# Kernel optimization log

Measured on AMD Instinct MI355X. Metric: run time of the kernel, lower is better.

The kernel has to match this reference:

```python
import jax, jax.numpy as jnp
import numpy as np

LN_EPS = 1e-5

def sin_emb(coords, dim):
    # coords [..., 3] -> [..., dim]; dim split evenly over 3 axes, sin/cos halves
    per_axis = dim // 3
    half = per_axis // 2
    freqs = jnp.exp(-jnp.log(10000.0) * jnp.arange(half, dtype=coords.dtype) / max(half - 1, 1))
    ang = coords[..., None] * freqs  # [..., 3, half]
    emb = jnp.concatenate([jnp.sin(ang), jnp.cos(ang)], axis=-1)  # [..., 3, per_axis]
    return emb.reshape(coords.shape[:-1] + (dim,))

def layernorm(x, g, b):
    mu = jnp.mean(x, axis=-1, keepdims=True)
    var = jnp.mean((x - mu) ** 2, axis=-1, keepdims=True)
    return (x - mu) * jax.lax.rsqrt(var + LN_EPS) * g + b

def point_mlp(x, w, b, g, be, act):
    h = layernorm(x @ w + b, g, be)
    return jax.nn.gelu(h, approximate=False) if act else h

def query_ball_point(radius, nsample, xyz):
    # xyz [B,N,3] -> idx [B,N,nsample] (pad with first in-ball index, PointNet++ style)
    N = xyz.shape[1]
    sq = jnp.sum((xyz[:, :, None, :] - xyz[:, None, :, :]) ** 2, axis=-1)  # [B,N,N]
    idx0 = jnp.where(sq > radius * radius, N, jnp.arange(N)[None, None, :])
    idx = jnp.sort(idx0, axis=-1)[:, :, :nsample]
    return jnp.where(idx == N, idx[:, :, :1], idx)

def index_points(points, idx):
    # points [B,N,C], idx [B,S,K] -> [B,S,K,C]
    return jax.vmap(lambda p, i: p[i])(points, idx)

def setup_inputs() -> dict:
    key = jax.random.key(0)
    ks = jax.random.split(key, 20)
    B, N, C_stem, C_tok = 4, 4096, 64, 256
    C_in = C_stem + 3 + 24 + 96  # 187
    w = lambda k, i, o: jax.random.normal(k, (i, o), jnp.float32) * 0.02
    inp = {
        'xyz': jax.random.uniform(ks[0], (B, N, 3), jnp.float32),
        'point_feature': jax.random.normal(ks[1], (B, N, C_stem), jnp.float32),
        # scene_point_mlp
        'w1': w(ks[2], C_in, C_tok), 'b1': jnp.zeros((C_tok,)), 'g1': jnp.ones((C_tok,)), 'be1': jnp.zeros((C_tok,)),
        'w2': w(ks[3], C_tok, C_tok), 'b2': jnp.zeros((C_tok,)), 'g2': jnp.ones((C_tok,)), 'be2': jnp.zeros((C_tok,)),
        # scene_projection
        'pw1': w(ks[4], C_tok, C_tok), 'pb1': jnp.zeros((C_tok,)), 'pg1': jnp.ones((C_tok,)), 'pbe1': jnp.zeros((C_tok,)),
        'pw2': w(ks[5], C_tok, C_tok), 'pb2': jnp.zeros((C_tok,)), 'pg2': jnp.ones((C_tok,)), 'pbe2': jnp.zeros((C_tok,)),
    }
    return inp

def reference(xyz, point_feature, w1, b1, g1, be1, w2, b2, g2, be2,
              pw1, pb1, pg1, pbe1, pw2, pb2, pg2, pbe2):
    radius, K = 0.16, 32
    idx = query_ball_point(radius, K, xyz)                     # [B,N,K]
    grouped_xyz = index_points(xyz, idx)                       # [B,N,K,3]
    grouped_feature = index_points(point_feature, idx)         # [B,N,K,Cs]
    relative_xyz = grouped_xyz - xyz[:, :, None, :]            # [B,N,K,3]
    relative_position = sin_emb(relative_xyz, 24)              # [B,N,K,24]
    absolute_position = sin_emb(xyz, 96)                       # [B,N,96]
    B, N = xyz.shape[0], xyz.shape[1]
    absolute_position = jnp.broadcast_to(absolute_position[:, :, None, :], (B, N, K, 96))
    grouped_input = jnp.concatenate(
        (grouped_feature, relative_xyz, relative_position, absolute_position), axis=-1)
    h = point_mlp(grouped_input, w1, b1, g1, be1, True)
    h = point_mlp(h, w2, b2, g2, be2, False)
    scene_point_feature = jnp.max(h, axis=2)                   # [B,N,C]
    pooled = jnp.max(scene_point_feature, axis=1, keepdims=True)  # [B,1,C]
    t = point_mlp(pooled, pw1, pb1, pg1, pbe1, True)
    global_scene_token = point_mlp(t, pw2, pb2, pg2, pbe2, False)
    return global_scene_token
```

## Files before the change

### kernel.cpp

```cpp
#include <hip/hip_runtime.h>
#include <hip/hip_bf16.h>
#include <math.h>


#define LN_EPS 1e-5f

typedef __attribute__((ext_vector_type(8))) short bf16x8;
typedef __attribute__((ext_vector_type(4))) float f32x4;
typedef __attribute__((ext_vector_type(2))) unsigned int u32x2;
typedef __attribute__((ext_vector_type(4))) unsigned int u32x4;

#if __has_builtin(__builtin_amdgcn_rcpf)
#define FRCP(x) __builtin_amdgcn_rcpf(x)
#else
#define FRCP(x) (1.0f / (x))
#endif

__device__ __forceinline__ unsigned short f2bf(float f) {
    unsigned int x = __float_as_uint(f);
    return (unsigned short)((x + 0x7FFFu + ((x >> 16) & 1u)) >> 16);
}
__device__ __forceinline__ unsigned int pack2(float a, float b) {
    union { __hip_bfloat162 h; unsigned int u; } cvt;
    cvt.h = __float22bfloat162_rn(make_float2(a, b));
    return cvt.u;
}
__device__ __forceinline__ unsigned int fenc(float f) {
    unsigned int u = __float_as_uint(f);
    return (u & 0x80000000u) ? ~u : (u | 0x80000000u);
}
__device__ __forceinline__ float fdec(unsigned int u) {
    return __uint_as_float((u & 0x80000000u) ? (u & 0x7FFFFFFFu) : ~u);
}
__device__ __forceinline__ float gelu_fast(float x) {
    float x2 = x * x;
    float u = x * fmaf(0.0356774081f, x2, 0.7978845608f);
    float e = exp2f(u * -2.8853900818f);
    float r = FRCP(e + 1.0f);
    return x * r;
}
template<int CTRL>
__device__ __forceinline__ float dppadd(float s) {
    int v = __builtin_amdgcn_update_dpp(0, __float_as_int(s), CTRL, 0xF, 0xF, true);
    return s + __int_as_float(v);
}
__device__ __forceinline__ float rowsum16(float x) {
    x = dppadd<0x128>(x);
    x = dppadd<0x124>(x);
    x = dppadd<0x122>(x);
    x = dppadd<0x121>(x);
    return x;
}

__global__ __launch_bounds__(256) void k_prep(
    const float* __restrict__ w1, const float* __restrict__ w2,
    unsigned short* __restrict__ w2T, unsigned short* __restrict__ w1aT,
    unsigned short* __restrict__ w1cT, unsigned short* __restrict__ w1bT,
    unsigned int* __restrict__ pooled_r)
{
    int t = threadIdx.x, blk = blockIdx.x;
    if (blk < 16) {
        __shared__ unsigned short tile[64][65];
        int tr = blk >> 2, tc = blk & 3;
        #pragma unroll
        for (int rr = 0; rr < 16; ++rr) {
            int kl = rr * 4 + (t >> 6), nl = t & 63;
            tile[kl][nl] = f2bf(w2[(size_t)(tr * 64 + kl) * 256 + tc * 64 + nl]);
        }
        __syncthreads();
        #pragma unroll
        for (int rr = 0; rr < 16; ++rr) {
            int nl = rr * 4 + (t >> 6), kp = t & 63;
            int kl = (kp & 3) * 16 + (kp >> 2);
            w2T[(size_t)(tc * 64 + nl) * 256 + tr * 64 + kp] = tile[kl][nl];
        }
    } else if (blk < 20) {
        __shared__ unsigned short tile[64][65];
        int tc = blk - 16;
        #pragma unroll
        for (int rr = 0; rr < 16; ++rr) {
            int kl = rr * 4 + (t >> 6), nl = t & 63;
            tile[kl][nl] = f2bf(w1[(size_t)kl * 256 + tc * 64 + nl]);
        }
        __syncthreads();
        #pragma unroll
        for (int rr = 0; rr < 16; ++rr) {
            int nl = rr * 4 + (t >> 6), kl = t & 63;
            w1aT[(size_t)(tc * 64 + nl) * 64 + kl] = tile[kl][nl];
        }
    } else if (blk < 28) {
        __shared__ unsigned short tile[64][65];
        int idx = blk - 20;
        int tr2 = idx >> 2, tc = idx & 3;
        #pragma unroll
        for (int rr = 0; rr < 16; ++rr) {
            int kl = rr * 4 + (t >> 6), nl = t & 63;
            int k = tr2 * 64 + kl;
            float v = 0.f;
            if (k < 96) v = w1[(size_t)(91 + k) * 256 + tc * 64 + nl];
            tile[kl][nl] = f2bf(v);
        }
        __syncthreads();
        #pragma unroll
        for (int rr = 0; rr < 16; ++rr) {
            int nl = rr * 4 + (t >> 6), kl = t & 63;
            int k = tr2 * 64 + kl;
            if (k < 96)
                w1cT[(size_t)(tc * 64 + nl) * 96 + k] = tile[kl][nl];
        }
    } else if (blk == 28) {
        int n = t;
        #pragma unroll
        for (int k = 0; k < 32; ++k) {
            unsigned short v = 0;
            if (k < 27) v = f2bf(w1[(size_t)(64 + k) * 256 + n]);
            w1bT[(size_t)n * 32 + k] = v;
        }
    } else {
        unsigned int idv = fenc(-1e19f);
        for (int q = t; q < 32768; q += 256) pooled_r[q] = idv;
    }
}

__global__ __launch_bounds__(256) void k_pre(
    const float* __restrict__ xyz, const float* __restrict__ pf,
    const unsigned short* __restrict__ w1aT, const unsigned short* __restrict__ w1cT,
    const float* __restrict__ b1,
    float* __restrict__ U_p, float* __restrict__ V_p)
{
    __shared__ __align__(16) unsigned short ptile[16 * 72];
    __shared__ __align__(16) unsigned short etile[16 * 104];
    int tid = threadIdx.x, wv = tid >> 6, lane = tid & 63;
    int lo16 = lane & 15, quad = lane >> 4;
    int rows0 = blockIdx.x * 16;

    {
        int r = tid >> 4, seg = tid & 15;
        f32x4 v = *(const f32x4*)(pf + (size_t)(rows0 + r) * 64 + seg * 4);
        u32x2 o; o.x = pack2(v.x, v.y); o.y = pack2(v.z, v.w);
        *(u32x2*)&ptile[r * 72 + seg * 4] = o;
    }
    #pragma unroll
    for (int q = 0; q < 3; ++q) {
        int item = q * 256 + tid;
        int r = item / 48, pr = item - 48 * r;
        float vals[2];
        #pragma unroll
        for (int qq = 0; qq < 2; ++qq) {
            int cc = pr * 2 + qq;
            int a = cc >> 5, wI = cc & 31;
            int jf = (wI < 16) ? wI : (wI - 16);
            float coord = xyz[(size_t)(rows0 + r) * 3 + a];
            float fr = __expf(-0.61402269146507894f * (float)jf);
            float ang = coord * fr;
            vals[qq] = (wI < 16) ? __sinf(ang) : __cosf(ang);
        }
        *(unsigned int*)&etile[r * 104 + 2 * pr] = pack2(vals[0], vals[1]);
    }
    __syncthreads();

    f32x4 acc[4];
    #pragma unroll
    for (int nt = 0; nt < 4; ++nt) acc[nt] = (f32x4){0.f, 0.f, 0.f, 0.f};
    #pragma unroll
    for (int ks = 0; ks < 2; ++ks) {
        bf16x8 afr = *(const bf16x8*)&ptile[lo16 * 72 + ks * 32 + quad * 8];
        #pragma unroll
        for (int nt = 0; nt < 4; ++nt) {
            int n = wv * 64 + nt * 16 + lo16;
            bf16x8 bfr = *(const bf16x8*)&w1aT[(size_t)n * 64 + ks * 32 + quad * 8];
            acc[nt] = __builtin_amdgcn_mfma_f32_16x16x32_bf16(afr, bfr, acc[nt], 0, 0, 0);
        }
    }
    #pragma unroll
    for (int reg = 0; reg < 4; ++reg) {
        f32x4 o = {acc[0][reg], acc[1][reg], acc[2][reg], acc[3][reg]};
        *(f32x4*)&U_p[(size_t)(rows0 + quad * 4 + reg) * 256 + wv * 64 + lo16 * 4] = o;
    }

    {
        float b1f[4];
        #pragma unroll
        for (int nt = 0; nt < 4; ++nt) b1f[nt] = b1[wv * 64 + nt * 16 + lo16];
        #pragma unroll
        for (int nt = 0; nt < 4; ++nt)
            #pragma unroll
            for (int reg = 0; reg < 4; ++reg) acc[nt][reg] = b1f[nt];
    }
    #pragma unroll
    for (int ks = 0; ks < 3; ++ks) {
        bf16x8 afr = *(const bf16x8*)&etile[lo16 * 104 + ks * 32 + quad * 8];
        #pragma unroll
        for (int nt = 0; nt < 4; ++nt) {
            int n = wv * 64 + nt * 16 + lo16;
            bf16x8 bfr = *(const bf16x8*)&w1cT[(size_t)n * 96 + ks * 32 + quad * 8];
            acc[nt] = __builtin_amdgcn_mfma_f32_16x16x32_bf16(afr, bfr, acc[nt], 0, 0, 0);
        }
    }
    #pragma unroll
    for (int reg = 0; reg < 4; ++reg) {
        f32x4 o = {acc[0][reg], acc[1][reg], acc[2][reg], acc[3][reg]};
        *(f32x4*)&V_p[(size_t)(rows0 + quad * 4 + reg) * 256 + wv * 64 + lo16 * 4] = o;
    }
}

__global__ __launch_bounds__(512, 4) void k_main(
    const float* __restrict__ xyz,
    const unsigned short* __restrict__ w1bT, const unsigned short* __restrict__ w2T,
    const float* __restrict__ U_p, const float* __restrict__ V_p,
    const float* __restrict__ g1, const float* __restrict__ be1,
    const float* __restrict__ b2, const float* __restrict__ g2,
    const float* __restrict__ be2,
    unsigned int* __restrict__ pooled_r)
{
    __shared__ __align__(16) unsigned short smem[128 * 264];
    __shared__ unsigned long long bmask[4][64];
    __shared__ int   idxs[128];
    __shared__ float ctr[4][3];
    __shared__ float reds[128][4][2];
    __shared__ float musig[128][2];
    __shared__ unsigned int pool_s[256];
    unsigned short* rels = smem;
    unsigned short* h1s  = smem;

    const int N = 4096;
    int tid = threadIdx.x, wv = tid >> 6, lane = tid & 63;
    int lo16 = lane & 15, quad = lane >> 4;
    int wvM = wv >> 2, wvN = wv & 3;
    int b = blockIdx.x & 3;
    int i0 = (blockIdx.x >> 2) * 4;
    int rep = (blockIdx.x >> 2) & 31;
    size_t base = (size_t)b * N;
    const float* xb = xyz + base * 3;

    bf16x8 bfrR[4];
    #pragma unroll
    for (int nt = 0; nt < 4; ++nt) {
        int n = wvN * 64 + nt * 16 + lo16;
        bfrR[nt] = *(const bf16x8*)&w1bT[(size_t)n * 32 + quad * 8];
    }

    if (tid < 256) pool_s[tid] = fenc(-1e19f);
    if (tid < 12) { int p = tid / 3, a = tid - 3 * p; ctr[p][a] = xb[(i0 + p) * 3 + a]; }
    const double r2d = 0.16 * 0.16;
    float T = (float)r2d;
    if ((double)T > r2d) T = __uint_as_float(__float_as_uint(T) - 1u);
    {
        f32x4 cA = *(const f32x4*)(xb + (size_t)i0 * 3);
        f32x4 cB = *(const f32x4*)(xb + (size_t)i0 * 3 + 4);
        f32x4 cC = *(const f32x4*)(xb + (size_t)i0 * 3 + 8);
        float cx0 = cA.x, cy0 = cA.y, cz0 = cA.z;
        float cx1 = cA.w, cy1 = cB.x, cz1 = cB.y;
        float cx2 = cB.z, cy2 = cB.w, cz2 = cC.x;
        float cx3 = cC.y, cy3 = cC.z, cz3 = cC.w;
        #pragma unroll 2
        for (int i = 0; i < 8; ++i) {
            int chunk = wv * 8 + i;
            int j = chunk * 64 + lane;
            const float* pp = xb + (size_t)j * 3;
            float px = pp[0], py = pp[1], pz = pp[2];
            float dx0 = __fsub_rn(px, cx0), dy0 = __fsub_rn(py, cy0), dz0 = __fsub_rn(pz, cz0);
            float sq0 = __fadd_rn(__fadd_rn(__fmul_rn(dx0, dx0), __fmul_rn(dy0, dy0)),
                                  __fmul_rn(dz0, dz0));
            unsigned long long m0 = __ballot(sq0 <= T);
            float dx1 = __fsub_rn(px, cx1), dy1 = __fsub_rn(py, cy1), dz1 = __fsub_rn(pz, cz1);
            float sq1 = __fadd_rn(__fadd_rn(__fmul_rn(dx1, dx1), __fmul_rn(dy1, dy1)),
                                  __fmul_rn(dz1, dz1));
            unsigned long long m1 = __ballot(sq1 <= T);
            float dx2 = __fsub_rn(px, cx2), dy2 = __fsub_rn(py, cy2), dz2 = __fsub_rn(pz, cz2);
            float sq2 = __fadd_rn(__fadd_rn(__fmul_rn(dx2, dx2), __fmul_rn(dy2, dy2)),
                                  __fmul_rn(dz2, dz2));
            unsigned long long m2 = __ballot(sq2 <= T);
            float dx3 = __fsub_rn(px, cx3), dy3 = __fsub_rn(py, cy3), dz3 = __fsub_rn(pz, cz3);
            float sq3 = __fadd_rn(__fadd_rn(__fmul_rn(dx3, dx3), __fmul_rn(dy3, dy3)),
                                  __fmul_rn(dz3, dz3));
            unsigned long long m3 = __ballot(sq3 <= T);
            if (lane == 0) {
                bmask[0][chunk] = m0; bmask[1][chunk] = m1;
                bmask[2][chunk] = m2; bmask[3][chunk] = m3;
            }
        }
    }
    __syncthreads();
    if (wv < 4) {
        int p = wv;
        unsigned long long m = bmask[p][lane];
        int c = __popcll(m);
        int inc = c;
        #pragma unroll
        for (int d = 1; d <= 32; d <<= 1) {
            int v = __shfl_up(inc, d);
            if (lane >= d) inc += v;
        }
        int exc = inc - c;
        int total = __shfl(inc, 63);
        unsigned long long lm = __ballot(m != 0ull);
        int fl = __ffsll(lm) - 1;
        unsigned long long mf = (unsigned long long)__shfl((long long)m, fl);
        int firstj = fl * 64 + __ffsll(mf) - 1;
        unsigned long long mm = m;
        int t = 0;
        while (mm != 0ull && (exc + t) < 32) {
            int bpos = __ffsll(mm) - 1;
            idxs[p * 32 + exc + t] = lane * 64 + bpos;
            mm &= mm - 1; ++t;
        }
        if (lane >= total && lane < 32) idxs[p * 32 + lane] = firstj;
    }
    __syncthreads();

    {
        int r = tid & 127, part = tid >> 7;
        int p = r >> 5;
        int j = idxs[r];
        float rx = xb[j * 3]     - ctr[p][0];
        float ry = xb[j * 3 + 1] - ctr[p][1];
        float rz = xb[j * 3 + 2] - ctr[p][2];
        unsigned short* arow = &rels[r * 40];
        if (part == 0) {
            *(unsigned int*)&arow[0] = pack2(rx, ry);
            arow[2] = f2bf(rz);
            arow[27] = 0;
            *(u32x2*)&arow[28] = (u32x2){0u, 0u};
        } else {
            int a = part - 1;
            float cv = (a == 0) ? rx : ((a == 1) ? ry : rz);
            const float fr4[4] = {1.f, 0.046415888336127774f,
                                  0.0021544346900318843f, 1e-4f};
            float sn[4], cs[4];
            #pragma unroll
            for (int tt = 0; tt < 4; ++tt) {
                float ang = cv * fr4[tt];
                sn[tt] = __sinf(ang); cs[tt] = __cosf(ang);
            }
            arow[3 + a * 8 + 0] = f2bf(sn[0]); arow[3 + a * 8 + 1] = f2bf(sn[1]);
            arow[3 + a * 8 + 2] = f2bf(sn[2]); arow[3 + a * 8 + 3] = f2bf(sn[3]);
            arow[3 + a * 8 + 4] = f2bf(cs[0]); arow[3 + a * 8 + 5] = f2bf(cs[1]);
            arow[3 + a * 8 + 6] = f2bf(cs[2]); arow[3 + a * 8 + 7] = f2bf(cs[3]);
        }
    }
    __syncthreads();

    const int arow0 = wvM * 64;
    f32x4 acc[4][4];
    #pragma unroll
    for (int mt = 0; mt < 4; ++mt) {
        int cl = wvM * 2 + (mt >> 1);
        f32x4 vv = *(const f32x4*)&V_p[(size_t)(base + i0 + cl) * 256 + wvN * 64 + lo16 * 4];
        #pragma unroll
        for (int reg = 0; reg < 4; ++reg) {
            int r = arow0 + mt * 16 + quad * 4 + reg;
            int j = idxs[r];
            f32x4 uu = *(const f32x4*)&U_p[(size_t)(base + j) * 256 + wvN * 64 + lo16 * 4];
            #pragma unroll
            for (int nt = 0; nt < 4; ++nt) acc[mt][nt][reg] = uu[nt] + vv[nt];
        }
    }
    #pragma unroll
    for (int mt = 0; mt < 4; ++mt) {
        bf16x8 afr = *(const bf16x8*)&rels[(arow0 + mt * 16 + lo16) * 40 + quad * 8];
        #pragma unroll
        for (int nt = 0; nt < 4; ++nt)
            acc[mt][nt] = __builtin_amdgcn_mfma_f32_16x16x32_bf16(
                afr, bfrR[nt], acc[mt][nt], 0, 0, 0);
    }

    #pragma unroll
    for (int mt = 0; mt < 4; ++mt) {
        #pragma unroll
        for (int reg = 0; reg < 4; ++reg) {
            float s1 = 0.f, s2 = 0.f;
            #pragma unroll
            for (int nt = 0; nt < 4; ++nt) { float v = acc[mt][nt][reg]; s1 += v; s2 = fmaf(v, v, s2); }
            s1 = rowsum16(s1); s2 = rowsum16(s2);
            if (lo16 == 0) {
                int r = arow0 + mt * 16 + quad * 4 + reg;
                reds[r][wvN][0] = s1; reds[r][wvN][1] = s2;
            }
        }
    }
    __syncthreads();
    if (tid < 128) {
        int r = tid;
        float s1 = reds[r][0][0] + reds[r][1][0] + reds[r][2][0] + reds[r][3][0];
        float s2 = reds[r][0][1] + reds[r][1][1] + reds[r][2][1] + reds[r][3][1];
        float mu = s1 * (1.f / 256.f);
        float var = fmaxf(s2 * (1.f / 256.f) - mu * mu, 0.f);
        musig[r][0] = mu; musig[r][1] = rsqrtf(var + LN_EPS);
    }
    __syncthreads();
    {
        float g1f[4], be1f[4];
        #pragma unroll
        for (int nt = 0; nt < 4; ++nt) {
            int n = wvN * 64 + nt * 16 + lo16;
            g1f[nt] = g1[n]; be1f[nt] = be1[n];
        }
        #pragma unroll
        for (int mt = 0; mt < 4; ++mt) {
            #pragma unroll
            for (int reg = 0; reg < 4; ++reg) {
                int r = arow0 + mt * 16 + quad * 4 + reg;
                float mu = musig[r][0], rs = musig[r][1];
                float v0 = gelu_fast(fmaf((acc[mt][0][reg] - mu) * rs, g1f[0], be1f[0]));
                float v1 = gelu_fast(fmaf((acc[mt][1][reg] - mu) * rs, g1f[1], be1f[1]));
                float v2 = gelu_fast(fmaf((acc[mt][2][reg] - mu) * rs, g1f[2], be1f[2]));
                float v3 = gelu_fast(fmaf((acc[mt][3][reg] - mu) * rs, g1f[3], be1f[3]));
                u32x2 w; w.x = pack2(v0, v1); w.y = pack2(v2, v3);
                *(u32x2*)&h1s[r * 264 + wvN * 64 + lo16 * 4] = w;
            }
        }
    }
    __syncthreads();

    {
        float b2f[4];
        #pragma unroll
        for (int nt = 0; nt < 4; ++nt) b2f[nt] = b2[wvN * 64 + nt * 16 + lo16];
        #pragma unroll
        for (int mt = 0; mt < 4; ++mt)
            #pragma unroll
            for (int nt = 0; nt < 4; ++nt)
                #pragma unroll
                for (int reg = 0; reg < 4; ++reg) acc[mt][nt][reg] = b2f[nt];
    }
    for (int ks = 0; ks < 8; ++ks) {
        bf16x8 bfr[4], afr[4];
        #pragma unroll
        for (int nt = 0; nt < 4; ++nt) {
            int n = wvN * 64 + nt * 16 + lo16;
            bfr[nt] = *(const bf16x8*)&w2T[(size_t)n * 256 + ks * 32 + quad * 8];
        }
        #pragma unroll
        for (int mt = 0; mt < 4; ++mt)
            afr[mt] = *(const bf16x8*)&h1s[(arow0 + mt * 16 + lo16) * 264 + ks * 32 + quad * 8];
        #pragma unroll
        for (int mt = 0; mt < 4; ++mt)
            #pragma unroll
            for (int nt = 0; nt < 4; ++nt)
                acc[mt][nt] = __builtin_amdgcn_mfma_f32_16x16x32_bf16(
                    afr[mt], bfr[nt], acc[mt][nt], 0, 0, 0);
    }

    {
        #pragma unroll
        for (int mt = 0; mt < 4; ++mt) {
            #pragma unroll
            for (int reg = 0; reg < 4; ++reg) {
                float s1 = 0.f, s2 = 0.f;
                #pragma unroll
                for (int nt = 0; nt < 4; ++nt) { float v = acc[mt][nt][reg]; s1 += v; s2 = fmaf(v, v, s2); }
                s1 = rowsum16(s1); s2 = rowsum16(s2);
                if (lo16 == 0) {
                    int r = arow0 + mt * 16 + quad * 4 + reg;
                    reds[r][wvN][0] = s1; reds[r][wvN][1] = s2;
                }
            }
        }
        __syncthreads();
        if (tid < 128) {
            int r = tid;
            float s1 = reds[r][0][0] + reds[r][1][0] + reds[r][2][0] + reds[r][3][0];
            float s2 = reds[r][0][1] + reds[r][1][1] + reds[r][2][1] + reds[r][3][1];
            float mu = s1 * (1.f / 256.f);
            float var = fmaxf(s2 * (1.f / 256.f) - mu * mu, 0.f);
            musig[r][0] = mu; musig[r][1] = rsqrtf(var + LN_EPS);
        }
        __syncthreads();

        float g2f[4], be2f[4];
        #pragma unroll
        for (int nt = 0; nt < 4; ++nt) {
            int n = wvN * 64 + nt * 16 + lo16;
            g2f[nt] = g2[n]; be2f[nt] = be2[n];
        }
        float mx[4] = {-1e30f, -1e30f, -1e30f, -1e30f};
        #pragma unroll
        for (int mt = 0; mt < 4; ++mt) {
            #pragma unroll
            for (int reg = 0; reg < 4; ++reg) {
                int r = arow0 + mt * 16 + quad * 4 + reg;
                float mu = musig[r][0], rs = musig[r][1];
                #pragma unroll
                for (int nt = 0; nt < 4; ++nt) {
                    float v = fmaf((acc[mt][nt][reg] - mu) * rs, g2f[nt], be2f[nt]);
                    mx[nt] = fmaxf(mx[nt], v);
                }
            }
        }
        #pragma unroll
        for (int nt = 0; nt < 4; ++nt) {
            mx[nt] = fmaxf(mx[nt], __shfl_xor(mx[nt], 16));
            mx[nt] = fmaxf(mx[nt], __shfl_xor(mx[nt], 32));
        }
        if (quad == 0) {
            #pragma unroll
            for (int nt = 0; nt < 4; ++nt)
                atomicMax(&pool_s[wvN * 64 + nt * 16 + lo16], fenc(mx[nt]));
        }
    }
    __syncthreads();
    if (tid < 256)
        atomicMax(pooled_r + rep * 1024 + b * 256 + tid, pool_s[tid]);
}

__global__ __launch_bounds__(256) void k_final(
    const unsigned int* __restrict__ pooled_r,
    const float* __restrict__ pw1, const float* __restrict__ pb1,
    const float* __restrict__ pg1, const float* __restrict__ pbe1,
    const float* __restrict__ pw2, const float* __restrict__ pb2,
    const float* __restrict__ pg2, const float* __restrict__ pbe2,
    float* __restrict__ out)
{
    __shared__ float xw[256], xh[256];
    __shared__ float lred[2][4];
    int tid = threadIdx.x, wv = tid >> 6;
    int bb = blockIdx.x;

    {
        unsigned int mv = pooled_r[bb * 256 + tid];
        #pragma unroll
        for (int r = 1; r < 32; ++r) {
            unsigned int v = pooled_r[r * 1024 + bb * 256 + tid];
            mv = (v > mv) ? v : mv;
        }
        xw[tid] = fdec(mv);
    }
    __syncthreads();

    float a1 = pb1[tid];
    #pragma unroll 8
    for (int k = 0; k < 256; ++k)
        a1 = fmaf(xw[k], pw1[(size_t)k * 256 + tid], a1);
    float s1 = a1, s2 = a1 * a1;
    s1 = rowsum16(s1); s2 = rowsum16(s2);
    s1 += __shfl_xor(s1, 16); s2 += __shfl_xor(s2, 16);
    s1 += __shfl_xor(s1, 32); s2 += __shfl_xor(s2, 32);
    if ((tid & 63) == 0) { lred[0][wv] = s1; lred[1][wv] = s2; }
    __syncthreads();
    s1 = lred[0][0] + lred[0][1] + lred[0][2] + lred[0][3];
    s2 = lred[1][0] + lred[1][1] + lred[1][2] + lred[1][3];
    float mu = s1 * (1.f / 256.f);
    float rs = rsqrtf(fmaxf(s2 * (1.f / 256.f) - mu * mu, 0.f) + LN_EPS);
    xh[tid] = gelu_fast(fmaf((a1 - mu) * rs, pg1[tid], pbe1[tid]));
    __syncthreads();

    float a2 = pb2[tid];
    #pragma unroll 8
    for (int k = 0; k < 256; ++k)
        a2 = fmaf(xh[k], pw2[(size_t)k * 256 + tid], a2);
    s1 = a2; s2 = a2 * a2;
    s1 = rowsum16(s1); s2 = rowsum16(s2);
    s1 += __shfl_xor(s1, 16); s2 += __shfl_xor(s2, 16);
    s1 += __shfl_xor(s1, 32); s2 += __shfl_xor(s2, 32);
    if ((tid & 63) == 0) { lred[0][wv] = s1; lred[1][wv] = s2; }
    __syncthreads();
    s1 = lred[0][0] + lred[0][1] + lred[0][2] + lred[0][3];
    s2 = lred[1][0] + lred[1][1] + lred[1][2] + lred[1][3];
    mu = s1 * (1.f / 256.f);
    rs = rsqrtf(fmaxf(s2 * (1.f / 256.f) - mu * mu, 0.f) + LN_EPS);
    out[bb * 256 + tid] = fmaf((a2 - mu) * rs, pg2[tid], pbe2[tid]);
}

extern "C" void kernel_launch(void* const* d_in, const int* in_sizes, int n_in,
                              void* d_out, int out_size, void* d_ws, size_t ws_size,
                              hipStream_t stream)
{
    char* ws = (char*)d_ws;
    unsigned short* w2T      = (unsigned short*)ws;
    unsigned short* w1aT     = (unsigned short*)(ws + (128u << 10));
    unsigned short* w1cT     = (unsigned short*)(ws + (160u << 10));
    unsigned short* w1bT     = (unsigned short*)(ws + (208u << 10));
    unsigned int*   pooled_r = (unsigned int*)(ws + (224u << 10));
    float*          U_p      = (float*)(ws + (512u << 10));
    float*          V_p      = (float*)(ws + (512u << 10) + (16u << 20));

    const float* xyz = (const float*)d_in[0];
    const float* pf  = (const float*)d_in[1];
    const float* w1  = (const float*)d_in[2];
    const float* b1  = (const float*)d_in[3];

    k_prep<<<30, 256, 0, stream>>>(w1, (const float*)d_in[6],
                                   w2T, w1aT, w1cT, w1bT, pooled_r);
    k_pre<<<1024, 256, 0, stream>>>(xyz, pf, w1aT, w1cT, b1, U_p, V_p);
    k_main<<<4096, 512, 0, stream>>>(xyz, w1bT, w2T, U_p, V_p,
                                     (const float*)d_in[4], (const float*)d_in[5],
                                     (const float*)d_in[7], (const float*)d_in[8],
                                     (const float*)d_in[9], pooled_r);
    k_final<<<4, 256, 0, stream>>>(pooled_r,
                                   (const float*)d_in[10], (const float*)d_in[11],
                                   (const float*)d_in[12], (const float*)d_in[13],
                                   (const float*)d_in[14], (const float*)d_in[15],
                                   (const float*)d_in[16], (const float*)d_in[17],
                                   (float*)d_out);
}
```

Before: 390.1 us.

## Use packed f32x2 math in ball query and LN epilogues; move weight prep into k_pre

Rewrites the ball-query distance computation and the layernorm/GELU epilogues of k_main with two-wide float vectors, so the compiler can emit packed FP32 instructions (v_pk_fma/mul/add) and halve the VALU instruction count. It also moves the w2 transpose, the w1b packing and the pooled buffer initialisation out of k_prep into 18 extra blocks appended to k_pre, shrinking the dependent prep kernel. Risks include register pressure from the vector packing and slightly different rounding, since the distance math no longer uses explicit _rn intrinsics.

```diff
diff --git a/kernel.cpp b/kernel.cpp
--- a/kernel.cpp
+++ b/kernel.cpp
@@ -7,6 +7,7 @@
 
 typedef __attribute__((ext_vector_type(8))) short bf16x8;
 typedef __attribute__((ext_vector_type(4))) float f32x4;
+typedef __attribute__((ext_vector_type(2))) float f32x2;
 typedef __attribute__((ext_vector_type(2))) unsigned int u32x2;
 typedef __attribute__((ext_vector_type(4))) unsigned int u32x4;
 
@@ -15,6 +16,17 @@
 #else
 #define FRCP(x) (1.0f / (x))
 #endif
+
+__device__ __forceinline__ f32x2 pk_add(f32x2 a, f32x2 b) { return a + b; }
+__device__ __forceinline__ f32x2 pk_sub(f32x2 a, f32x2 b) { return a - b; }
+__device__ __forceinline__ f32x2 pk_mul(f32x2 a, f32x2 b) { return a * b; }
+__device__ __forceinline__ f32x2 pk_fma(f32x2 a, f32x2 b, f32x2 c) {
+#if __has_builtin(__builtin_elementwise_fma)
+    return __builtin_elementwise_fma(a, b, c);
+#else
+    f32x2 d; d.x = fmaf(a.x, b.x, c.x); d.y = fmaf(a.y, b.y, c.y); return d;
+#endif
+}
 
 __device__ __forceinline__ unsigned short f2bf(float f) {
     unsigned int x = __float_as_uint(f);
@@ -39,6 +51,20 @@
     float r = FRCP(e + 1.0f);
     return x * r;
 }
+__device__ __forceinline__ f32x2 gelu2(f32x2 x) {
+    const f32x2 C0 = {0.0356774081f, 0.0356774081f};
+    const f32x2 C1 = {0.7978845608f, 0.7978845608f};
+    const f32x2 M  = {-2.8853900818f, -2.8853900818f};
+    const f32x2 ONE = {1.f, 1.f};
+    f32x2 x2 = pk_mul(x, x);
+    f32x2 t  = pk_fma(C0, x2, C1);
+    f32x2 u  = pk_mul(x, t);
+    f32x2 m  = pk_mul(u, M);
+    f32x2 e; e.x = exp2f(m.x); e.y = exp2f(m.y);
+    f32x2 ep = pk_add(e, ONE);
+    f32x2 r; r.x = FRCP(ep.x); r.y = FRCP(ep.y);
+    return pk_mul(x, r);
+}
 template<int CTRL>
 __device__ __forceinline__ float dppadd(float s) {
     int v = __builtin_amdgcn_update_dpp(0, __float_as_int(s), CTRL, 0xF, 0xF, true);
@@ -53,30 +79,13 @@
 }
 
 __global__ __launch_bounds__(256) void k_prep(
-    const float* __restrict__ w1, const float* __restrict__ w2,
-    unsigned short* __restrict__ w2T, unsigned short* __restrict__ w1aT,
-    unsigned short* __restrict__ w1cT, unsigned short* __restrict__ w1bT,
-    unsigned int* __restrict__ pooled_r)
+    const float* __restrict__ w1,
+    unsigned short* __restrict__ w1aT, unsigned short* __restrict__ w1cT)
 {
     int t = threadIdx.x, blk = blockIdx.x;
-    if (blk < 16) {
+    if (blk < 4) {
         __shared__ unsigned short tile[64][65];
-        int tr = blk >> 2, tc = blk & 3;
-        #pragma unroll
-        for (int rr = 0; rr < 16; ++rr) {
-            int kl = rr * 4 + (t >> 6), nl = t & 63;
-            tile[kl][nl] = f2bf(w2[(size_t)(tr * 64 + kl) * 256 + tc * 64 + nl]);
-        }
-        __syncthreads();
-        #pragma unroll
-        for (int rr = 0; rr < 16; ++rr) {
-            int nl = rr * 4 + (t >> 6), kp = t & 63;
-            int kl = (kp & 3) * 16 + (kp >> 2);
-            w2T[(size_t)(tc * 64 + nl) * 256 + tr * 64 + kp] = tile[kl][nl];
-        }
-    } else if (blk < 20) {
-        __shared__ unsigned short tile[64][65];
-        int tc = blk - 16;
+        int tc = blk;
         #pragma unroll
         for (int rr = 0; rr < 16; ++rr) {
             int kl = rr * 4 + (t >> 6), nl = t & 63;
@@ -88,9 +97,9 @@
             int nl = rr * 4 + (t >> 6), kl = t & 63;
             w1aT[(size_t)(tc * 64 + nl) * 64 + kl] = tile[kl][nl];
         }
-    } else if (blk < 28) {
+    } else {
         __shared__ unsigned short tile[64][65];
-        int idx = blk - 20;
+        int idx = blk - 4;
         int tr2 = idx >> 2, tc = idx & 3;
         #pragma unroll
         for (int rr = 0; rr < 16; ++rr) {
@@ -108,32 +117,57 @@
             if (k < 96)
                 w1cT[(size_t)(tc * 64 + nl) * 96 + k] = tile[kl][nl];
         }
-    } else if (blk == 28) {
-        int n = t;
-        #pragma unroll
-        for (int k = 0; k < 32; ++k) {
-            unsigned short v = 0;
-            if (k < 27) v = f2bf(w1[(size_t)(64 + k) * 256 + n]);
-            w1bT[(size_t)n * 32 + k] = v;
-        }
-    } else {
-        unsigned int idv = fenc(-1e19f);
-        for (int q = t; q < 32768; q += 256) pooled_r[q] = idv;
     }
 }
 
 __global__ __launch_bounds__(256) void k_pre(
     const float* __restrict__ xyz, const float* __restrict__ pf,
+    const float* __restrict__ w1, const float* __restrict__ w2,
     const unsigned short* __restrict__ w1aT, const unsigned short* __restrict__ w1cT,
     const float* __restrict__ b1,
-    float* __restrict__ U_p, float* __restrict__ V_p)
+    float* __restrict__ U_p, float* __restrict__ V_p,
+    unsigned short* __restrict__ w2T, unsigned short* __restrict__ w1bT,
+    unsigned int* __restrict__ pooled_r)
 {
     __shared__ __align__(16) unsigned short ptile[16 * 72];
     __shared__ __align__(16) unsigned short etile[16 * 104];
+    __shared__ unsigned short tile[64][65];
     int tid = threadIdx.x, wv = tid >> 6, lane = tid & 63;
     int lo16 = lane & 15, quad = lane >> 4;
+
+    if (blockIdx.x >= 1024) {
+        int blk = blockIdx.x - 1024;
+        int t = tid;
+        if (blk < 16) {
+            int tr = blk >> 2, tc = blk & 3;
+            #pragma unroll
+            for (int rr = 0; rr < 16; ++rr) {
+                int kl = rr * 4 + (t >> 6), nl = t & 63;
+                tile[kl][nl] = f2bf(w2[(size_t)(tr * 64 + kl) * 256 + tc * 64 + nl]);
+            }
+            __syncthreads();
+            #pragma unroll
+            for (int rr = 0; rr < 16; ++rr) {
+                int nl = rr * 4 + (t >> 6), kp = t & 63;
+                int kl = (kp & 3) * 16 + (kp >> 2);
+                w2T[(size_t)(tc * 64 + nl) * 256 + tr * 64 + kp] = tile[kl][nl];
+            }
+        } else if (blk == 16) {
+            int n = t;
+            #pragma unroll
+            for (int k = 0; k < 32; ++k) {
+                unsigned short v = 0;
+                if (k < 27) v = f2bf(w1[(size_t)(64 + k) * 256 + n]);
+                w1bT[(size_t)n * 32 + k] = v;
+            }
+        } else {
+            unsigned int idv = fenc(-1e19f);
+            for (int q = t; q < 32768; q += 256) pooled_r[q] = idv;
+        }
+        return;
+    }
+
     int rows0 = blockIdx.x * 16;
-
     {
         int r = tid >> 4, seg = tid & 15;
         f32x4 v = *(const f32x4*)(pf + (size_t)(rows0 + r) * 64 + seg * 4);
@@ -249,32 +283,25 @@
         f32x4 cA = *(const f32x4*)(xb + (size_t)i0 * 3);
         f32x4 cB = *(const f32x4*)(xb + (size_t)i0 * 3 + 4);
         f32x4 cC = *(const f32x4*)(xb + (size_t)i0 * 3 + 8);
-        float cx0 = cA.x, cy0 = cA.y, cz0 = cA.z;
-        float cx1 = cA.w, cy1 = cB.x, cz1 = cB.y;
-        float cx2 = cB.z, cy2 = cB.w, cz2 = cC.x;
-        float cx3 = cC.y, cy3 = cC.z, cz3 = cC.w;
+        f32x2 cx01 = {cA.x, cA.w}, cy01 = {cA.y, cB.x}, cz01 = {cA.z, cB.y};
+        f32x2 cx23 = {cB.z, cC.y}, cy23 = {cB.w, cC.z}, cz23 = {cC.x, cC.w};
         #pragma unroll 2
         for (int i = 0; i < 8; ++i) {
             int chunk = wv * 8 + i;
             int j = chunk * 64 + lane;
             const float* pp = xb + (size_t)j * 3;
             float px = pp[0], py = pp[1], pz = pp[2];
-            float dx0 = __fsub_rn(px, cx0), dy0 = __fsub_rn(py, cy0), dz0 = __fsub_rn(pz, cz0);
-            float sq0 = __fadd_rn(__fadd_rn(__fmul_rn(dx0, dx0), __fmul_rn(dy0, dy0)),
-                                  __fmul_rn(dz0, dz0));
-            unsigned long long m0 = __ballot(sq0 <= T);
-            float dx1 = __fsub_rn(px, cx1), dy1 = __fsub_rn(py, cy1), dz1 = __fsub_rn(pz, cz1);
-            float sq1 = __fadd_rn(__fadd_rn(__fmul_rn(dx1, dx1), __fmul_rn(dy1, dy1)),
-                                  __fmul_rn(dz1, dz1));
-            unsigned long long m1 = __ballot(sq1 <= T);
-            float dx2 = __fsub_rn(px, cx2), dy2 = __fsub_rn(py, cy2), dz2 = __fsub_rn(pz, cz2);
-            float sq2 = __fadd_rn(__fadd_rn(__fmul_rn(dx2, dx2), __fmul_rn(dy2, dy2)),
-                                  __fmul_rn(dz2, dz2));
-            unsigned long long m2 = __ballot(sq2 <= T);
-            float dx3 = __fsub_rn(px, cx3), dy3 = __fsub_rn(py, cy3), dz3 = __fsub_rn(pz, cz3);
-            float sq3 = __fadd_rn(__fadd_rn(__fmul_rn(dx3, dx3), __fmul_rn(dy3, dy3)),
-                                  __fmul_rn(dz3, dz3));
-            unsigned long long m3 = __ballot(sq3 <= T);
+            f32x2 pxx = {px, px}, pyy = {py, py}, pzz = {pz, pz};
+            f32x2 dx01 = pk_sub(pxx, cx01), dy01 = pk_sub(pyy, cy01), dz01 = pk_sub(pzz, cz01);
+            f32x2 sq01 = pk_add(pk_add(pk_mul(dx01, dx01), pk_mul(dy01, dy01)),
+                                pk_mul(dz01, dz01));
+            unsigned long long m0 = __ballot(sq01.x <= T);
+            unsigned long long m1 = __ballot(sq01.y <= T);
+            f32x2 dx23 = pk_sub(pxx, cx23), dy23 = pk_sub(pyy, cy23), dz23 = pk_sub(pzz, cz23);
+            f32x2 sq23 = pk_add(pk_add(pk_mul(dx23, dx23), pk_mul(dy23, dy23)),
+                                pk_mul(dz23, dz23));
+            unsigned long long m2 = __ballot(sq23.x <= T);
+            unsigned long long m3 = __ballot(sq23.y <= T);
             if (lane == 0) {
                 bmask[0][chunk] = m0; bmask[1][chunk] = m1;
                 bmask[2][chunk] = m2; bmask[3][chunk] = m3;
@@ -396,17 +423,22 @@
             int n = wvN * 64 + nt * 16 + lo16;
             g1f[nt] = g1[n]; be1f[nt] = be1[n];
         }
+        f32x2 g01 = {g1f[0], g1f[1]}, g23 = {g1f[2], g1f[3]};
+        f32x2 be01 = {be1f[0], be1f[1]}, be23 = {be1f[2], be1f[3]};
         #pragma unroll
         for (int mt = 0; mt < 4; ++mt) {
             #pragma unroll
             for (int reg = 0; reg < 4; ++reg) {
                 int r = arow0 + mt * 16 + quad * 4 + reg;
                 float mu = musig[r][0], rs = musig[r][1];
-                float v0 = gelu_fast(fmaf((acc[mt][0][reg] - mu) * rs, g1f[0], be1f[0]));
-                float v1 = gelu_fast(fmaf((acc[mt][1][reg] - mu) * rs, g1f[1], be1f[1]));
-                float v2 = gelu_fast(fmaf((acc[mt][2][reg] - mu) * rs, g1f[2], be1f[2]));
-                float v3 = gelu_fast(fmaf((acc[mt][3][reg] - mu) * rs, g1f[3], be1f[3]));
-                u32x2 w; w.x = pack2(v0, v1); w.y = pack2(v2, v3);
+                f32x2 mu2 = {mu, mu}, rs2 = {rs, rs};
+                f32x2 a01 = {acc[mt][0][reg], acc[mt][1][reg]};
+                f32x2 a23 = {acc[mt][2][reg], acc[mt][3][reg]};
+                f32x2 h01 = pk_fma(pk_mul(pk_sub(a01, mu2), rs2), g01, be01);
+                f32x2 h23 = pk_fma(pk_mul(pk_sub(a23, mu2), rs2), g23, be23);
+                f32x2 o01 = gelu2(h01);
+                f32x2 o23 = gelu2(h23);
+                u32x2 w; w.x = pack2(o01.x, o01.y); w.y = pack2(o23.x, o23.y);
                 *(u32x2*)&h1s[r * 264 + wvN * 64 + lo16 * 4] = w;
             }
         }
@@ -474,6 +506,8 @@
             int n = wvN * 64 + nt * 16 + lo16;
             g2f[nt] = g2[n]; be2f[nt] = be2[n];
         }
+        f32x2 g01 = {g2f[0], g2f[1]}, g23 = {g2f[2], g2f[3]};
+        f32x2 be01 = {be2f[0], be2f[1]}, be23 = {be2f[2], be2f[3]};
         float mx[4] = {-1e30f, -1e30f, -1e30f, -1e30f};
         #pragma unroll
         for (int mt = 0; mt < 4; ++mt) {
@@ -481,11 +515,15 @@
             for (int reg = 0; reg < 4; ++reg) {
                 int r = arow0 + mt * 16 + quad * 4 + reg;
                 float mu = musig[r][0], rs = musig[r][1];
-                #pragma unroll
-                for (int nt = 0; nt < 4; ++nt) {
-                    float v = fmaf((acc[mt][nt][reg] - mu) * rs, g2f[nt], be2f[nt]);
-                    mx[nt] = fmaxf(mx[nt], v);
-                }
+                f32x2 mu2 = {mu, mu}, rs2 = {rs, rs};
+                f32x2 a01 = {acc[mt][0][reg], acc[mt][1][reg]};
+                f32x2 a23 = {acc[mt][2][reg], acc[mt][3][reg]};
+                f32x2 v01 = pk_fma(pk_mul(pk_sub(a01, mu2), rs2), g01, be01);
+                f32x2 v23 = pk_fma(pk_mul(pk_sub(a23, mu2), rs2), g23, be23);
+                mx[0] = fmaxf(mx[0], v01.x);
+                mx[1] = fmaxf(mx[1], v01.y);
+                mx[2] = fmaxf(mx[2], v23.x);
+                mx[3] = fmaxf(mx[3], v23.y);
             }
         }
         #pragma unroll
@@ -579,10 +617,11 @@
     const float* pf  = (const float*)d_in[1];
     const float* w1  = (const float*)d_in[2];
     const float* b1  = (const float*)d_in[3];
-
-    k_prep<<<30, 256, 0, stream>>>(w1, (const float*)d_in[6],
-                                   w2T, w1aT, w1cT, w1bT, pooled_r);
-    k_pre<<<1024, 256, 0, stream>>>(xyz, pf, w1aT, w1cT, b1, U_p, V_p);
+    const float* w2  = (const float*)d_in[6];
+
+    k_prep<<<12, 256, 0, stream>>>(w1, w1aT, w1cT);
+    k_pre<<<1042, 256, 0, stream>>>(xyz, pf, w1, w2, w1aT, w1cT, b1,
+                                    U_p, V_p, w2T, w1bT, pooled_r);
     k_main<<<4096, 512, 0, stream>>>(xyz, w1bT, w2T, U_p, V_p,
                                      (const float*)d_in[4], (const float*)d_in[5],
                                      (const float*)d_in[7], (const float*)d_in[8],
```

Result: slower. 410.7 us (+5.3%).
